# Kernel tuning notes

Hardware: AMD Instinct MI355X
Metric: run time of the kernel (lower is better)

Reference implementation:

```python
import jax, jax.numpy as jnp
import numpy as np

EMB = 768
N_HEADS = 12
HEAD_DIM = EMB // N_HEADS
EPS = 1e-5


def _gelu_tanh(x):
    c = jnp.sqrt(jnp.asarray(2.0 / jnp.pi, x.dtype))
    return 0.5 * x * (1.0 + jnp.tanh(c * (x + 0.044715 * x ** 3)))


def _layernorm(x, scale, shift):
    mean = jnp.mean(x, axis=-1, keepdims=True)
    var = jnp.mean((x - mean) ** 2, axis=-1, keepdims=True)
    return (x - mean) / jnp.sqrt(var + EPS) * scale + shift


def setup_inputs() -> dict:
    key = jax.random.key(0)
    ks = jax.random.split(key, 8)
    s = 0.02  # GPT-2 style init scale
    x = jax.random.normal(ks[0], (8, 1024, EMB), dtype=jnp.float32)
    # torch Linear weights are (out, in); no biases (qkv_bias=False everywhere)
    wq = jax.random.normal(ks[1], (EMB, EMB), dtype=jnp.float32) * s
    wk = jax.random.normal(ks[2], (EMB, EMB), dtype=jnp.float32) * s
    wv = jax.random.normal(ks[3], (EMB, EMB), dtype=jnp.float32) * s
    wo = jax.random.normal(ks[4], (EMB, EMB), dtype=jnp.float32) * s
    w1 = jax.random.normal(ks[5], (4 * EMB, EMB), dtype=jnp.float32) * s
    w2 = jax.random.normal(ks[6], (EMB, 4 * EMB), dtype=jnp.float32) * s
    ln1_scale = jnp.ones((EMB,), jnp.float32)
    ln1_shift = jnp.zeros((EMB,), jnp.float32)
    ln2_scale = jnp.ones((EMB,), jnp.float32)
    ln2_shift = jnp.zeros((EMB,), jnp.float32)
    return dict(x=x, wq=wq, wk=wk, wv=wv, wo=wo, w1=w1, w2=w2,
                ln1_scale=ln1_scale, ln1_shift=ln1_shift,
                ln2_scale=ln2_scale, ln2_shift=ln2_shift)


def reference(x, wq, wk, wv, wo, w1, w2, ln1_scale, ln1_shift, ln2_scale, ln2_shift):
    B, T, E = x.shape
    # --- attention sublayer (pre-LN) ---
    h = _layernorm(x, ln1_scale, ln1_shift)
    q = (h @ wq.T).reshape(B, T, N_HEADS, HEAD_DIM).transpose(0, 2, 1, 3)
    k = (h @ wk.T).reshape(B, T, N_HEADS, HEAD_DIM).transpose(0, 2, 1, 3)
    v = (h @ wv.T).reshape(B, T, N_HEADS, HEAD_DIM).transpose(0, 2, 1, 3)
    scores = jnp.einsum('bhqd,bhkd->bhqk', q, k)  # [B,H,T,T]
    causal = jnp.tril(jnp.ones((T, T), dtype=bool))
    scores = jnp.where(causal, scores, -jnp.inf)
    attn = jax.nn.softmax(scores / np.sqrt(HEAD_DIM), axis=-1)
    ctx = jnp.einsum('bhqk,bhkd->bhqd', attn, v)
    ctx = ctx.transpose(0, 2, 1, 3).reshape(B, T, E)
    x = x + ctx @ wo.T
    # --- FFN sublayer (pre-LN) ---
    h = _layernorm(x, ln2_scale, ln2_shift)
    h = _gelu_tanh(h @ w1.T) @ w2.T
    return x + h
```

## Files before the change

kernel.cpp:

```cpp
#include <hip/hip_runtime.h>
#include <hip/hip_bf16.h>
#include <cstdint>

#define EMB    768
#define NHEADS 12
#define HDIM   64
#define SEQ    1024
#define BATCH  8
#define MROWS  (BATCH*SEQ)
#define FFN    3072
#define W2E    (EMB*EMB)
#define W4E    (FFN*EMB)

typedef __bf16 bf16_t;
typedef bf16_t bf16x8 __attribute__((ext_vector_type(8)));
typedef float  f32x4  __attribute__((ext_vector_type(4)));

__device__ __forceinline__ float b2f(unsigned short u) {
    union { unsigned int i; float f; } t; t.i = ((unsigned int)u) << 16; return t.f;
}
__device__ __forceinline__ unsigned short f2b(float f) {
    union { float f; unsigned int i; } t; t.f = f;
    unsigned int lsb = (t.i >> 16) & 1u;
    t.i += 0x7fffu + lsb;
    return (unsigned short)(t.i >> 16);
}
__device__ __forceinline__ float gelu_f(float x) {
    float u = 0.7978845608028654f * (x + 0.044715f * x * x * x);
    return x * (1.f / (1.f + __expf(-2.f * u)));
}
__device__ __forceinline__ float fexp2(float x) {
#if defined(__has_builtin)
#if __has_builtin(__builtin_amdgcn_exp2f)
    return __builtin_amdgcn_exp2f(x);
#else
    return exp2f(x);
#endif
#else
    return exp2f(x);
#endif
}

#if defined(__has_builtin)
#if __has_builtin(__builtin_amdgcn_global_load_lds)
#define HAS_GLL 1
#endif
#endif
#ifndef HAS_GLL
#define HAS_GLL 0
#endif

__device__ __forceinline__ void gll16(const unsigned short* g, unsigned short* lds_wave_base) {
#if HAS_GLL
    __builtin_amdgcn_global_load_lds(
        (const __attribute__((address_space(1))) unsigned int*)g,
        (__attribute__((address_space(3))) unsigned int*)lds_wave_base, 16, 0, 0);
#endif
}
__device__ __forceinline__ void stage16(const unsigned short* g, unsigned short* lds_wave_base, int lane) {
#if HAS_GLL
    __builtin_amdgcn_global_load_lds(
        (const __attribute__((address_space(1))) unsigned int*)g,
        (__attribute__((address_space(3))) unsigned int*)lds_wave_base, 16, 0, 0);
#else
    *reinterpret_cast<int4*>(lds_wave_base + lane * 8) = *reinterpret_cast<const int4*>(g);
#endif
}

__device__ __forceinline__ int4 load8(const void* src, size_t eoff, bool f32) {
    if (f32) {
        const float4* p = reinterpret_cast<const float4*>((const float*)src + eoff);
        float4 a = p[0], b = p[1];
        union { unsigned short u[8]; int4 v; } r;
        r.u[0] = f2b(a.x); r.u[1] = f2b(a.y); r.u[2] = f2b(a.z); r.u[3] = f2b(a.w);
        r.u[4] = f2b(b.x); r.u[5] = f2b(b.y); r.u[6] = f2b(b.z); r.u[7] = f2b(b.w);
        return r.v;
    }
    return *reinterpret_cast<const int4*>((const unsigned short*)src + eoff);
}
__device__ __forceinline__ float4 load4f(const void* src, size_t eoff, bool f32) {
    if (f32) return *reinterpret_cast<const float4*>((const float*)src + eoff);
    ushort4 u = *reinterpret_cast<const ushort4*>((const unsigned short*)src + eoff);
    float4 r; r.x = b2f(u.x); r.y = b2f(u.y); r.z = b2f(u.z); r.w = b2f(u.w);
    return r;
}

struct DetectArgs { const unsigned short* p[11]; int n[11]; };

__global__ __launch_bounds__(256) void detect_all(DetectArgs a, int* __restrict__ flags) {
    __shared__ int cnt;
    if (threadIdx.x == 0) cnt = 0;
    __syncthreads();
    const unsigned short* src = a.p[blockIdx.x];
    int npairs = a.n[blockIdx.x] / 2;
    if (npairs > 4096) npairs = 4096;
    int local = 0;
    for (int p = threadIdx.x; p < npairs; p += 256) {
        unsigned short u0 = src[2 * p], u1 = src[2 * p + 1];
        int e0 = (u0 >> 7) & 0xFF;
        bool insane0 = (e0 == 0xFF) || (u0 != 0 && (e0 < 96 || e0 > 159));
        bool zpat    = (u0 == 0 && u1 != 0);
        if (insane0 || zpat) ++local;
    }
    atomicAdd(&cnt, local);
    __syncthreads();
    if (threadIdx.x == 0) flags[blockIdx.x] = (cnt * 8 > npairs) ? 1 : 0;
}

__global__ __launch_bounds__(256) void cvt_adapt(
        const void* __restrict__ src, unsigned short* __restrict__ dst,
        int n, const int* __restrict__ flag) {
    int i = blockIdx.x * 256 + threadIdx.x;
    if (i * 4 >= n) return;
    if (*flag) {
        float4 f = reinterpret_cast<const float4*>(src)[i];
        ushort4 o;
        o.x = f2b(f.x); o.y = f2b(f.y); o.z = f2b(f.z); o.w = f2b(f.w);
        reinterpret_cast<ushort4*>(dst)[i] = o;
    } else {
        reinterpret_cast<ushort4*>(dst)[i] = reinterpret_cast<const ushort4*>(src)[i];
    }
}

struct CvtArgs {
    const void* src[6];
    unsigned short* dst[6];
    int n[6];
    int blkoff[7];
    const int* F;
    int fidx[6];
};
__global__ __launch_bounds__(256) void cvt_weights(CvtArgs a) {
    int b = blockIdx.x, seg = 0;
    #pragma unroll
    for (int s = 0; s < 6; ++s) if (b >= a.blkoff[s + 1]) seg = s + 1;
    int i = (b - a.blkoff[seg]) * 256 + threadIdx.x;
    if (i * 4 >= a.n[seg]) return;
    if (a.F[a.fidx[seg]]) {
        float4 f = reinterpret_cast<const float4*>(a.src[seg])[i];
        ushort4 o;
        o.x = f2b(f.x); o.y = f2b(f.y); o.z = f2b(f.z); o.w = f2b(f.w);
        reinterpret_cast<ushort4*>(a.dst[seg])[i] = o;
    } else {
        reinterpret_cast<ushort4*>(a.dst[seg])[i] =
            reinterpret_cast<const ushort4*>(a.src[seg])[i];
    }
}

__global__ __launch_bounds__(256) void reduce2_kernel(
        const float* __restrict__ P, const unsigned short* __restrict__ resid,
        float* __restrict__ out, int n4) {
    int i = blockIdx.x * 256 + threadIdx.x;
    if (i >= n4) return;
    float4 a = reinterpret_cast<const float4*>(P)[i];
    float4 b = reinterpret_cast<const float4*>(P + (size_t)MROWS * EMB)[i];
    ushort4 r = reinterpret_cast<const ushort4*>(resid)[i];
    float4 o;
    o.x = a.x + b.x + b2f(r.x);
    o.y = a.y + b.y + b2f(r.y);
    o.z = a.z + b.z + b2f(r.z);
    o.w = a.w + b.w + b2f(r.w);
    reinterpret_cast<float4*>(out)[i] = o;
}

__global__ __launch_bounds__(256) void ln_kernel(
        const void* __restrict__ x,     const int* __restrict__ fx,
        const void* __restrict__ scale, const int* __restrict__ fsc,
        const void* __restrict__ shift, const int* __restrict__ fsh,
        unsigned short* __restrict__ out) {
    const bool xf = fx && *fx, scf = fsc && *fsc, shf = fsh && *fsh;
    int wave = threadIdx.x >> 6;
    int lane = threadIdx.x & 63;
    int row  = blockIdx.x * 4 + wave;
    const size_t rbase = (size_t)row * EMB;
    float v[12];
    float s = 0.f, s2 = 0.f;
    #pragma unroll
    for (int i = 0; i < 3; ++i) {
        float4 a = load4f(x, rbase + i * 256 + lane * 4, xf);
        v[i*4+0] = a.x; v[i*4+1] = a.y; v[i*4+2] = a.z; v[i*4+3] = a.w;
        s  += a.x + a.y + a.z + a.w;
        s2 += a.x*a.x + a.y*a.y + a.z*a.z + a.w*a.w;
    }
    #pragma unroll
    for (int off = 1; off < 64; off <<= 1) {
        s  += __shfl_xor(s,  off);
        s2 += __shfl_xor(s2, off);
    }
    float mean = s * (1.f / EMB);
    float var  = fmaxf(s2 * (1.f / EMB) - mean * mean, 0.f);
    float rstd = rsqrtf(var + 1e-5f);
    unsigned short* orow = out + rbase;
    #pragma unroll
    for (int i = 0; i < 3; ++i) {
        float4 sc = load4f(scale, i * 256 + lane * 4, scf);
        float4 sh = load4f(shift, i * 256 + lane * 4, shf);
        ushort4 o;
        o.x = f2b((v[i*4+0] - mean) * rstd * sc.x + sh.x);
        o.y = f2b((v[i*4+1] - mean) * rstd * sc.y + sh.y);
        o.z = f2b((v[i*4+2] - mean) * rstd * sc.z + sh.z);
        o.w = f2b((v[i*4+3] - mean) * rstd * sc.w + sh.w);
        *reinterpret_cast<ushort4*>(orow + i * 256 + lane * 4) = o;
    }
}

template<bool GELU, bool RESID, bool OUTF32>
__global__ __launch_bounds__(256) void gemm_lds(
        const unsigned short* __restrict__ A,
        const unsigned short* __restrict__ W,
        const void* R, const int* __restrict__ fR, size_t rOff,
        void* C, int M, int N, int K, int lda, int ldw) {
    constexpr int BK = 32;
    __shared__ __align__(16) unsigned short sA[128 * BK];
    __shared__ __align__(16) unsigned short sB[128 * BK];
    const int m0 = blockIdx.x * 128, n0 = blockIdx.y * 128;
    const int kz = blockIdx.z;
    const int t = threadIdx.x, wave = t >> 6, lane = t & 63;
    const int wrow = (wave >> 1) * 64, wcol = (wave & 1) * 64;
    const int quad = lane >> 4, lr = lane & 15;
    const int r0 = t >> 2;
    const int scg = (t & 3) ^ ((t >> 3) & 3);
    const int c0 = scg * 8;
    const int xq = quad ^ ((lr >> 1) & 3);
    const bool rf = fR && *fR;

    A += (size_t)kz * K;
    W += (size_t)kz * K;

    f32x4 acc[4][4];
    #pragma unroll
    for (int i = 0; i < 4; ++i)
        #pragma unroll
        for (int j = 0; j < 4; ++j)
            acc[i][j] = (f32x4){0.f, 0.f, 0.f, 0.f};

    const unsigned short* gA0 = A + (size_t)(m0 + r0) * lda + c0;
    const unsigned short* gA1 = A + (size_t)(m0 + 64 + r0) * lda + c0;
    const unsigned short* gB0 = W + (size_t)(n0 + r0) * ldw + c0;
    const unsigned short* gB1 = W + (size_t)(n0 + 64 + r0) * ldw + c0;
    unsigned short* lA0 = sA + wave * 512;
    unsigned short* lA1 = sA + 2048 + wave * 512;
    unsigned short* lB0 = sB + wave * 512;
    unsigned short* lB1 = sB + 2048 + wave * 512;

    for (int k0 = 0; k0 < K; k0 += BK) {
#if HAS_GLL
        gll16(gA0 + k0, lA0);
        gll16(gA1 + k0, lA1);
        gll16(gB0 + k0, lB0);
        gll16(gB1 + k0, lB1);
#else
        *reinterpret_cast<int4*>(sA + t * 8)        = *reinterpret_cast<const int4*>(gA0 + k0);
        *reinterpret_cast<int4*>(sA + 2048 + t * 8) = *reinterpret_cast<const int4*>(gA1 + k0);
        *reinterpret_cast<int4*>(sB + t * 8)        = *reinterpret_cast<const int4*>(gB0 + k0);
        *reinterpret_cast<int4*>(sB + 2048 + t * 8) = *reinterpret_cast<const int4*>(gB1 + k0);
#endif
        __syncthreads();
        bf16x8 af[4], bfv[4];
        #pragma unroll
        for (int i = 0; i < 4; ++i)
            af[i] = *reinterpret_cast<const bf16x8*>(
                sA + (wrow >> 6) * 2048 + (i * 16 + lr) * 32 + xq * 8);
        #pragma unroll
        for (int j = 0; j < 4; ++j)
            bfv[j] = *reinterpret_cast<const bf16x8*>(
                sB + (wcol >> 6) * 2048 + (j * 16 + lr) * 32 + xq * 8);
        #pragma unroll
        for (int i = 0; i < 4; ++i)
            #pragma unroll
            for (int j = 0; j < 4; ++j)
                acc[i][j] = __builtin_amdgcn_mfma_f32_16x16x32_bf16(af[i], bfv[j], acc[i][j], 0, 0, 0);
        __syncthreads();
    }

    float* Cf = (float*)C + (size_t)kz * M * N;
    #pragma unroll
    for (int i = 0; i < 4; ++i) {
        #pragma unroll
        for (int j = 0; j < 4; ++j) {
            #pragma unroll
            for (int r = 0; r < 4; ++r) {
                int row = m0 + wrow + i * 16 + quad * 4 + r;
                int col = n0 + wcol + j * 16 + lr;
                float val = acc[i][j][r];
                if (GELU) val = gelu_f(val);
                size_t idx = (size_t)row * N + col;
                if (RESID) {
                    float rv = rf ? ((const float*)R)[idx + rOff]
                                  : b2f(((const unsigned short*)R)[idx + rOff]);
                    val += rv;
                }
                if (OUTF32) Cf[idx] = val;
                else        ((unsigned short*)C)[idx] = f2b(val);
            }
        }
    }
}

template<bool GELU, bool RESID, bool OUTF32>
__global__ __launch_bounds__(256) void gemm_bt(
        const unsigned short* __restrict__ A,
        const void* __restrict__ W, const int* __restrict__ fW,
        const void* R, const int* __restrict__ fR, size_t rOff,
        void* C,
        int M, int N, int K) {
    const bool wf = fW && *fW;
    const bool rf = fR && *fR;
    constexpr int BK = 32, PAD = 8, LDW = BK + PAD;
    __shared__ __align__(16) unsigned short sA[128 * LDW];
    __shared__ __align__(16) unsigned short sB[128 * LDW];
    const int m0 = blockIdx.x * 128;
    const int n0 = blockIdx.y * 128;
    const int t    = threadIdx.x;
    const int wave = t >> 6, lane = t & 63;
    const int wrow = (wave >> 1) * 64, wcol = (wave & 1) * 64;
    const int quad = lane >> 4, lr = lane & 15;
    const int srow = t >> 2, scol = (t & 3) * 8;

    f32x4 acc[4][4];
    #pragma unroll
    for (int i = 0; i < 4; ++i)
        #pragma unroll
        for (int j = 0; j < 4; ++j)
            acc[i][j] = (f32x4){0.f, 0.f, 0.f, 0.f};

    const size_t aBase = (size_t)(m0 + srow) * K + scol;
    const size_t bBase = (size_t)(n0 + srow) * K + scol;

    for (int k0 = 0; k0 < K; k0 += BK) {
        int4 av0 = *reinterpret_cast<const int4*>(A + aBase + k0);
        int4 av1 = *reinterpret_cast<const int4*>(A + aBase + (size_t)64 * K + k0);
        int4 bv0 = load8(W, bBase + k0, wf);
        int4 bv1 = load8(W, bBase + (size_t)64 * K + k0, wf);
        *reinterpret_cast<int4*>(sA + srow * LDW + scol)        = av0;
        *reinterpret_cast<int4*>(sA + (srow + 64) * LDW + scol) = av1;
        *reinterpret_cast<int4*>(sB + srow * LDW + scol)        = bv0;
        *reinterpret_cast<int4*>(sB + (srow + 64) * LDW + scol) = bv1;
        __syncthreads();
        bf16x8 af[4], bfv[4];
        #pragma unroll
        for (int i = 0; i < 4; ++i)
            af[i] = *reinterpret_cast<const bf16x8*>(sA + (wrow + i * 16 + lr) * LDW + quad * 8);
        #pragma unroll
        for (int j = 0; j < 4; ++j)
            bfv[j] = *reinterpret_cast<const bf16x8*>(sB + (wcol + j * 16 + lr) * LDW + quad * 8);
        #pragma unroll
        for (int i = 0; i < 4; ++i)
            #pragma unroll
            for (int j = 0; j < 4; ++j)
                acc[i][j] = __builtin_amdgcn_mfma_f32_16x16x32_bf16(af[i], bfv[j], acc[i][j], 0, 0, 0);
        __syncthreads();
    }

    #pragma unroll
    for (int i = 0; i < 4; ++i) {
        #pragma unroll
        for (int j = 0; j < 4; ++j) {
            #pragma unroll
            for (int r = 0; r < 4; ++r) {
                int row = m0 + wrow + i * 16 + quad * 4 + r;
                int col = n0 + wcol + j * 16 + lr;
                float val = acc[i][j][r];
                if (GELU) val = gelu_f(val);
                size_t idx = (size_t)row * N + col;
                if (RESID) {
                    float rv = rf ? ((const float*)R)[idx + rOff]
                                  : b2f(((const unsigned short*)R)[idx + rOff]);
                    val += rv;
                }
                if (OUTF32) ((float*)C)[idx] = val;
                else        ((unsigned short*)C)[idx] = f2b(val);
            }
        }
    }
}

__global__ __launch_bounds__(256) void fattn_kernel(
        const unsigned short* __restrict__ q,
        const unsigned short* __restrict__ k,
        const unsigned short* __restrict__ v,
        int rs, unsigned short* __restrict__ ctx) {
    constexpr int VTP = 72;
    __shared__ __align__(16) unsigned short sK[2][64 * 64];
    __shared__ __align__(16) unsigned short Vt[2][64 * VTP];
    __shared__ __align__(16) unsigned short Pl[4][16 * VTP];
    const int tid  = threadIdx.x;
    const int wave = tid >> 6, lane = tid & 63;
    const int quad = lane >> 4, lr = lane & 15;
    const int NH   = gridDim.x >> 3;
    const int head = blockIdx.x % NH;
    const int pr   = blockIdx.x / NH;
    const int bb   = head / NHEADS, hd = head % NHEADS;
    const size_t seqbase = (size_t)bb * SEQ;
    constexpr float C2 = 0.18033688011112042f;

    const int krow0 = tid >> 3;
    const int dreal = ((tid & 7) * 8) ^ ((krow0 & 7) << 3);
    const int vrow = tid >> 2;
    const int vcol = (tid & 3) * 16;
    const int vxr  = vrow ^ ((tid & 3) << 4);
    const int kswz = (lr & 7) << 3;
    const int pswr = ((lr >> 2) & 3) << 3;
    unsigned short* Pw = Pl[wave];

    #pragma unroll
    for (int seg = 0; seg < 2; ++seg) {
        const int qt = seg == 0 ? (15 - pr) : pr;
        const int q0 = qt * 64 + wave * 16;

        bf16x8 aQ0, aQ1;
        {
            const unsigned short* qp = q + (seqbase + q0 + lr) * rs + hd * HDIM + quad * 8;
            aQ0 = *reinterpret_cast<const bf16x8*>(qp);
            aQ1 = *reinterpret_cast<const bf16x8*>(qp + 32);
        }

        f32x4 O[4];
        #pragma unroll
        for (int i = 0; i < 4; ++i) O[i] = (f32x4){0.f, 0.f, 0.f, 0.f};
        float mrow[4], lrow[4];
        #pragma unroll
        for (int r = 0; r < 4; ++r) { mrow[r] = -__builtin_inff(); lrow[r] = 0.f; }

        {
            const unsigned short* kp = k + (seqbase + krow0) * rs + hd * HDIM + dreal;
            stage16(kp,                   &sK[0][wave * 512],        lane);
            stage16(kp + (size_t)32 * rs, &sK[0][2048 + wave * 512], lane);
            const unsigned short* vp = v + (seqbase + vrow) * rs + hd * HDIM + vcol;
            union { int4 v4; unsigned short u[8]; } pa, pb;
            pa.v4 = *reinterpret_cast<const int4*>(vp);
            pb.v4 = *reinterpret_cast<const int4*>(vp + 8);
            #pragma unroll
            for (int e = 0; e < 8; ++e) Vt[0][(vcol + e) * VTP + vxr]     = pa.u[e];
            #pragma unroll
            for (int e = 0; e < 8; ++e) Vt[0][(vcol + 8 + e) * VTP + vxr] = pb.u[e];
        }
        __syncthreads();

        for (int kt = 0; kt <= qt; ++kt) {
            const int b = kt & 1;
            union { int4 v4; unsigned short u[8]; } ua, ub;
            if (kt < qt) {
                const unsigned short* kp = k + (seqbase + (size_t)(kt + 1) * 64 + krow0) * rs
                                         + hd * HDIM + dreal;
                stage16(kp,                   &sK[b ^ 1][wave * 512],        lane);
                stage16(kp + (size_t)32 * rs, &sK[b ^ 1][2048 + wave * 512], lane);
                const unsigned short* vp = v + (seqbase + (size_t)(kt + 1) * 64 + vrow) * rs
                                         + hd * HDIM + vcol;
                ua.v4 = *reinterpret_cast<const int4*>(vp);
                ub.v4 = *reinterpret_cast<const int4*>(vp + 8);
            }

            f32x4 S[4];
            #pragma unroll
            for (int sub = 0; sub < 4; ++sub) {
                const unsigned short* kr = &sK[b][(sub * 16 + lr) * 64];
                bf16x8 b0 = *reinterpret_cast<const bf16x8*>(kr + ((quad * 8) ^ kswz));
                bf16x8 b1 = *reinterpret_cast<const bf16x8*>(kr + ((32 + quad * 8) ^ kswz));
                f32x4 accS = (f32x4){0.f, 0.f, 0.f, 0.f};
                accS = __builtin_amdgcn_mfma_f32_16x16x32_bf16(aQ0, b0, accS, 0, 0, 0);
                accS = __builtin_amdgcn_mfma_f32_16x16x32_bf16(aQ1, b1, accS, 0, 0, 0);
                S[sub] = accS;
            }
            const bool diag = (kt == qt);
            #pragma unroll
            for (int sub = 0; sub < 4; ++sub) {
                const int kg = kt * 64 + sub * 16 + lr;
                #pragma unroll
                for (int r = 0; r < 4; ++r) {
                    float s = S[sub][r] * C2;
                    if (diag && kg > q0 + quad * 4 + r) s = -__builtin_inff();
                    S[sub][r] = s;
                }
            }
            float mnew[4], alpha[4];
            #pragma unroll
            for (int r = 0; r < 4; ++r) {
                float mx = fmaxf(fmaxf(S[0][r], S[1][r]), fmaxf(S[2][r], S[3][r]));
                #pragma unroll
                for (int m = 1; m < 16; m <<= 1) mx = fmaxf(mx, __shfl_xor(mx, m));
                mnew[r]  = fmaxf(mrow[r], mx);
                alpha[r] = fexp2(mrow[r] - mnew[r]);
                mrow[r]  = mnew[r];
            }
            float rsum[4] = {0.f, 0.f, 0.f, 0.f};
            #pragma unroll
            for (int sub = 0; sub < 4; ++sub)
                #pragma unroll
                for (int r = 0; r < 4; ++r) {
                    float p = fexp2(S[sub][r] - mnew[r]);
                    S[sub][r] = p;
                    rsum[r] += p;
                }
            #pragma unroll
            for (int r = 0; r < 4; ++r) {
                float rs2 = rsum[r];
                #pragma unroll
                for (int m = 1; m < 16; m <<= 1) rs2 += __shfl_xor(rs2, m);
                lrow[r] = lrow[r] * alpha[r] + rs2;
            }

            #pragma unroll
            for (int sub = 0; sub < 4; ++sub)
                #pragma unroll
                for (int r = 0; r < 4; ++r) {
                    bf16_t hv = (bf16_t)S[sub][r];
                    Pw[(quad * 4 + r) * VTP + ((sub * 16 + lr) ^ (quad << 3))] =
                        *reinterpret_cast<unsigned short*>(&hv);
                }
            if (kt < qt) {
                #pragma unroll
                for (int e = 0; e < 8; ++e) Vt[b ^ 1][(vcol + e) * VTP + vxr]     = ua.u[e];
                #pragma unroll
                for (int e = 0; e < 8; ++e) Vt[b ^ 1][(vcol + 8 + e) * VTP + vxr] = ub.u[e];
            }
            #pragma unroll
            for (int d = 0; d < 4; ++d)
                #pragma unroll
                for (int r = 0; r < 4; ++r)
                    O[d][r] *= alpha[r];

            #pragma unroll
            for (int c = 0; c < 2; ++c) {
                bf16x8 aP = *reinterpret_cast<const bf16x8*>(
                    &Pw[lr * VTP + ((c * 32 + quad * 8) ^ pswr)]);
                #pragma unroll
                for (int d = 0; d < 4; ++d) {
                    bf16x8 bV = *reinterpret_cast<const bf16x8*>(
                        &Vt[b][(d * 16 + lr) * VTP + ((c * 32 + quad * 8) ^ (d << 4))]);
                    O[d] = __builtin_amdgcn_mfma_f32_16x16x32_bf16(aP, bV, O[d], 0, 0, 0);
                }
            }
            __syncthreads();
        }

        #pragma unroll
        for (int r = 0; r < 4; ++r) {
            const float rinv = 1.f / lrow[r];
            const int qg = q0 + quad * 4 + r;
            unsigned short* crow = ctx + (seqbase + qg) * EMB + hd * HDIM;
            #pragma unroll
            for (int d = 0; d < 4; ++d)
                crow[d * 16 + lr] = f2b(O[d][r] * rinv);
        }
    }
}

extern "C" void kernel_launch(void* const* d_in, const int* in_sizes, int n_in,
                              void* d_out, int out_size, void* d_ws, size_t ws_size,
                              hipStream_t stream) {
    const void* x  = d_in[0];
    const void* wq = d_in[1], *wk = d_in[2], *wv = d_in[3], *wo = d_in[4];
    const void* w1 = d_in[5], *w2 = d_in[6];
    const void* g1 = d_in[7], *s1 = d_in[8], *g2 = d_in[9], *s2 = d_in[10];
    char* ws = (char*)d_ws;
    dim3 blk(256);

    int* F = (int*)ws;
    {
        DetectArgs da;
        for (int i = 0; i < 11; ++i) { da.p[i] = (const unsigned short*)d_in[i]; da.n[i] = in_sizes[i]; }
        detect_all<<<11, blk, 0, stream>>>(da, F);
    }

    const size_t SZE = (size_t)MROWS * EMB;
    const size_t SZB = SZE * 2;
    unsigned short* base = (unsigned short*)(ws + 256);
    dim3 g768(MROWS / 128, EMB / 128);

    const size_t FULLB = 256 + 2ULL * (2 * W4E) + 2ULL * (4 * W2E)
                       + 2ULL * ((size_t)MROWS * 2304) + 2 * SZB
                       + 2ULL * ((size_t)MROWS * FFN);
    const size_t FULLB2 = FULLB + 2ULL * SZE * 4;

    if (ws_size >= FULLB2) {
        unsigned short* w1b   = base;
        unsigned short* w2b   = w1b + W4E;
        unsigned short* wqkvb = w2b + W4E;
        unsigned short* wob   = wqkvb + 3 * W2E;
        unsigned short* P     = wob + W2E;
        unsigned short* B0    = P + (size_t)MROWS * 2304;
        unsigned short* B1    = B0 + SZE;
        unsigned short* G     = B1 + SZE;
        float*          PK    = (float*)(G + (size_t)MROWS * FFN);

        {
            CvtArgs ca;
            ca.src[0] = wq; ca.src[1] = wk; ca.src[2] = wv;
            ca.src[3] = wo; ca.src[4] = w1; ca.src[5] = w2;
            ca.dst[0] = wqkvb; ca.dst[1] = wqkvb + W2E; ca.dst[2] = wqkvb + 2 * W2E;
            ca.dst[3] = wob;   ca.dst[4] = w1b;         ca.dst[5] = w2b;
            ca.n[0] = ca.n[1] = ca.n[2] = ca.n[3] = W2E; ca.n[4] = ca.n[5] = W4E;
            int off = 0;
            for (int s = 0; s < 6; ++s) { ca.blkoff[s] = off; off += ca.n[s] / 1024; }
            ca.blkoff[6] = off;
            ca.F = F;
            ca.fidx[0] = 1; ca.fidx[1] = 2; ca.fidx[2] = 3;
            ca.fidx[3] = 4; ca.fidx[4] = 5; ca.fidx[5] = 6;
            cvt_weights<<<off, blk, 0, stream>>>(ca);
        }

        ln_kernel<<<MROWS / 4, blk, 0, stream>>>(x, F+0, g1, F+7, s1, F+8, B1);
        dim3 gqkv(MROWS / 128, 2304 / 128);
        gemm_lds<false, false, false><<<gqkv, blk, 0, stream>>>(B1, wqkvb, nullptr, nullptr, 0, P, MROWS, 2304, EMB, EMB, EMB);
        fattn_kernel<<<BATCH * NHEADS * 8, blk, 0, stream>>>(P, P + 768, P + 1536, 2304, B0);
        gemm_lds<false, true, false><<<g768, blk, 0, stream>>>(B0, wob, x, F+0, 0, B1, MROWS, EMB, EMB, EMB, EMB);
        ln_kernel<<<MROWS / 4, blk, 0, stream>>>(B1, nullptr, g2, F+9, s2, F+10, B0);
        dim3 gffn1(MROWS / 128, FFN / 128);
        gemm_lds<true, false, false><<<gffn1, blk, 0, stream>>>(B0, w1b, nullptr, nullptr, 0, G, MROWS, FFN, EMB, EMB, EMB);
        dim3 gsk(MROWS / 128, EMB / 128, 2);
        gemm_lds<false, false, true><<<gsk, blk, 0, stream>>>(G, w2b, nullptr, nullptr, 0, PK, MROWS, EMB, FFN / 2, FFN, FFN);
        reduce2_kernel<<<(SZE / 4 + 255) / 256, blk, 0, stream>>>(PK, B1, (float*)d_out, SZE / 4);
    } else if (ws_size >= FULLB) {
        unsigned short* w1b   = base;
        unsigned short* w2b   = w1b + W4E;
        unsigned short* wqkvb = w2b + W4E;
        unsigned short* wob   = wqkvb + 3 * W2E;
        unsigned short* P     = wob + W2E;
        unsigned short* B0    = P + (size_t)MROWS * 2304;
        unsigned short* B1    = B0 + SZE;
        unsigned short* G     = B1 + SZE;

        {
            CvtArgs ca;
            ca.src[0] = wq; ca.src[1] = wk; ca.src[2] = wv;
            ca.src[3] = wo; ca.src[4] = w1; ca.src[5] = w2;
            ca.dst[0] = wqkvb; ca.dst[1] = wqkvb + W2E; ca.dst[2] = wqkvb + 2 * W2E;
            ca.dst[3] = wob;   ca.dst[4] = w1b;         ca.dst[5] = w2b;
            ca.n[0] = ca.n[1] = ca.n[2] = ca.n[3] = W2E; ca.n[4] = ca.n[5] = W4E;
            int off = 0;
            for (int s = 0; s < 6; ++s) { ca.blkoff[s] = off; off += ca.n[s] / 1024; }
            ca.blkoff[6] = off;
            ca.F = F;
            ca.fidx[0] = 1; ca.fidx[1] = 2; ca.fidx[2] = 3;
            ca.fidx[3] = 4; ca.fidx[4] = 5; ca.fidx[5] = 6;
            cvt_weights<<<off, blk, 0, stream>>>(ca);
        }

        ln_kernel<<<MROWS / 4, blk, 0, stream>>>(x, F+0, g1, F+7, s1, F+8, B1);
        dim3 gqkv(MROWS / 128, 2304 / 128);
        gemm_lds<false, false, false><<<gqkv, blk, 0, stream>>>(B1, wqkvb, nullptr, nullptr, 0, P, MROWS, 2304, EMB, EMB, EMB);
        fattn_kernel<<<BATCH * NHEADS * 8, blk, 0, stream>>>(P, P + 768, P + 1536, 2304, B0);
        gemm_lds<false, true, false><<<g768, blk, 0, stream>>>(B0, wob, x, F+0, 0, B1, MROWS, EMB, EMB, EMB, EMB);
        ln_kernel<<<MROWS / 4, blk, 0, stream>>>(B1, nullptr, g2, F+9, s2, F+10, B0);
        dim3 gffn1(MROWS / 128, FFN / 128);
        gemm_lds<true, false, false><<<gffn1, blk, 0, stream>>>(B0, w1b, nullptr, nullptr, 0, G, MROWS, FFN, EMB, EMB, EMB);
        gemm_lds<false, true, true><<<g768, blk, 0, stream>>>(G, w2b, B1, nullptr, 0, d_out, MROWS, EMB, FFN, FFN, FFN);
    } else if (ws_size >= 256 + 4 * SZB) {
        unsigned short* B0 = base;
        unsigned short* B1 = B0 + SZE;
        unsigned short* B2 = B1 + SZE;
        unsigned short* B3 = B2 + SZE;
        ln_kernel<<<MROWS / 4, blk, 0, stream>>>(x, F+0, g1, F+7, s1, F+8, B0);
        gemm_bt<false, false, false><<<g768, blk, 0, stream>>>(B0, wq, F+1, nullptr, nullptr, 0, B1, MROWS, EMB, EMB);
        gemm_bt<false, false, false><<<g768, blk, 0, stream>>>(B0, wk, F+2, nullptr, nullptr, 0, B2, MROWS, EMB, EMB);
        gemm_bt<false, false, false><<<g768, blk, 0, stream>>>(B0, wv, F+3, nullptr, nullptr, 0, B3, MROWS, EMB, EMB);
        fattn_kernel<<<BATCH * NHEADS * 8, blk, 0, stream>>>(B1, B2, B3, EMB, B0);
        gemm_bt<false, true, false><<<g768, blk, 0, stream>>>(B0, wo, F+4, x, F+0, 0, B1, MROWS, EMB, EMB);
        ln_kernel<<<MROWS / 4, blk, 0, stream>>>(B1, nullptr, g2, F+9, s2, F+10, B2);
        dim3 c3072(2048 / 128, FFN / 128), c768(2048 / 128, EMB / 128);
        for (int c = 0; c < 4; ++c) {
            const size_t r0 = (size_t)c * 2048;
            gemm_bt<true, false, false><<<c3072, blk, 0, stream>>>(B2 + r0 * EMB, w1, F+5, nullptr, nullptr, 0, B3, 2048, FFN, EMB);
            gemm_bt<false, true, true><<<c768, blk, 0, stream>>>(B3, w2, F+6, B1 + r0 * EMB, nullptr, 0, (float*)d_out + r0 * EMB, 2048, EMB, FFN);
        }
    } else {
        unsigned short* hlow = (unsigned short*)d_out;
        unsigned short* x2up = (unsigned short*)d_out + SZE;
        unsigned short* wsQ = base;
        unsigned short* wsK = wsQ + (size_t)1024 * EMB;
        unsigned short* wsV = wsK + (size_t)1024 * EMB;
        unsigned short* wsC = wsV + (size_t)1024 * EMB;
        ln_kernel<<<MROWS / 4, blk, 0, stream>>>(x, F+0, g1, F+7, s1, F+8, hlow);
        dim3 q768(1024 / 128, EMB / 128);
        for (int grp = 0; grp < BATCH; ++grp) {
            const size_t r0 = (size_t)grp * 1024;
            gemm_bt<false, false, false><<<q768, blk, 0, stream>>>(hlow + r0 * EMB, wq, F+1, nullptr, nullptr, 0, wsQ, 1024, EMB, EMB);
            gemm_bt<false, false, false><<<q768, blk, 0, stream>>>(hlow + r0 * EMB, wk, F+2, nullptr, nullptr, 0, wsK, 1024, EMB, EMB);
            gemm_bt<false, false, false><<<q768, blk, 0, stream>>>(hlow + r0 * EMB, wv, F+3, nullptr, nullptr, 0, wsV, 1024, EMB, EMB);
            fattn_kernel<<<1 * NHEADS * 8, blk, 0, stream>>>(wsQ, wsK, wsV, EMB, wsC);
            gemm_bt<false, true, false><<<q768, blk, 0, stream>>>(wsC, wo, F+4, x, F+0, r0 * EMB, x2up + r0 * EMB, 1024, EMB, EMB);
        }
        unsigned short* xb = base;
        unsigned short* h2 = xb + (size_t)1024 * EMB;
        unsigned short* gb = h2 + (size_t)1024 * EMB;
        dim3 f3072(1024 / 128, FFN / 128), f768(1024 / 128, EMB / 128);
        for (int c = 0; c < BATCH; ++c) {
            const size_t r0 = (size_t)c * 1024;
            hipMemcpyAsync(xb, x2up + r0 * EMB, (size_t)1024 * EMB * 2,
                           hipMemcpyDeviceToDevice, stream);
            ln_kernel<<<1024 / 4, blk, 0, stream>>>(xb, nullptr, g2, F+9, s2, F+10, h2);
            gemm_bt<true, false, false><<<f3072, blk, 0, stream>>>(h2, w1, F+5, nullptr, nullptr, 0, gb, 1024, FFN, EMB);
            gemm_bt<false, true, true><<<f768, blk, 0, stream>>>(gb, w2, F+6, xb, nullptr, 0, (float*)d_out + r0 * EMB, 1024, EMB, FFN);
        }
    }
}
```

Before: 402.3 us.

## Double-buffer LDS in gemm_lds and use faster exp2/rcp GELU

Double-buffers the shared-memory tiles in gemm_lds so the next K-slice is prefetched (via global_load_lds when available) while MFMAs run on the current one, and drops one barrier per iteration. It also adds a launch-bounds occupancy hint, rewrites GELU with exp2 plus a hardware reciprocal, and uses the native bf16 conversion for stores. The extra LDS buffer doubles shared-memory use, and the single barrier per iteration may leave a race when the async LDS writes for the next slice are not waited on before the following compute.

Measured after the change: 390.6 us. -2.9%, faster.

```diff
diff --git a/kernel.cpp b/kernel.cpp
--- a/kernel.cpp
+++ b/kernel.cpp
@@ -25,10 +25,6 @@
     t.i += 0x7fffu + lsb;
     return (unsigned short)(t.i >> 16);
 }
-__device__ __forceinline__ float gelu_f(float x) {
-    float u = 0.7978845608028654f * (x + 0.044715f * x * x * x);
-    return x * (1.f / (1.f + __expf(-2.f * u)));
-}
 __device__ __forceinline__ float fexp2(float x) {
 #if defined(__has_builtin)
 #if __has_builtin(__builtin_amdgcn_exp2f)
@@ -39,6 +35,22 @@
 #else
     return exp2f(x);
 #endif
+}
+__device__ __forceinline__ float frcp(float x) {
+#if defined(__has_builtin)
+#if __has_builtin(__builtin_amdgcn_rcpf)
+    return __builtin_amdgcn_rcpf(x);
+#else
+    return 1.f / x;
+#endif
+#else
+    return 1.f / x;
+#endif
+}
+__device__ __forceinline__ float gelu_f(float x) {
+    float x2 = x * x;
+    float u  = x * __builtin_fmaf(x2, -0.10294823f, -2.3022082f);
+    return x * frcp(1.f + fexp2(u));
 }
 
 #if defined(__has_builtin)
@@ -205,17 +217,18 @@
 }
 
 template<bool GELU, bool RESID, bool OUTF32>
-__global__ __launch_bounds__(256) void gemm_lds(
+__global__ __launch_bounds__(256, 3) void gemm_lds(
         const unsigned short* __restrict__ A,
         const unsigned short* __restrict__ W,
         const void* R, const int* __restrict__ fR, size_t rOff,
         void* C, int M, int N, int K, int lda, int ldw) {
     constexpr int BK = 32;
-    __shared__ __align__(16) unsigned short sA[128 * BK];
-    __shared__ __align__(16) unsigned short sB[128 * BK];
+    __shared__ __align__(16) unsigned short sA[2][128 * BK];
+    __shared__ __align__(16) unsigned short sB[2][128 * BK];
     const int m0 = blockIdx.x * 128, n0 = blockIdx.y * 128;
     const int kz = blockIdx.z;
-    const int t = threadIdx.x, wave = t >> 6, lane = t & 63;
+    const int t = threadIdx.x, wave = t >> 6;
+    const int lane = t & 63;
     const int wrow = (wave >> 1) * 64, wcol = (wave & 1) * 64;
     const int quad = lane >> 4, lr = lane & 15;
     const int r0 = t >> 2;
@@ -238,39 +251,53 @@
     const unsigned short* gA1 = A + (size_t)(m0 + 64 + r0) * lda + c0;
     const unsigned short* gB0 = W + (size_t)(n0 + r0) * ldw + c0;
     const unsigned short* gB1 = W + (size_t)(n0 + 64 + r0) * ldw + c0;
-    unsigned short* lA0 = sA + wave * 512;
-    unsigned short* lA1 = sA + 2048 + wave * 512;
-    unsigned short* lB0 = sB + wave * 512;
-    unsigned short* lB1 = sB + 2048 + wave * 512;
-
+
+#if HAS_GLL
+    gll16(gA0, sA[0] + wave * 512);
+    gll16(gA1, sA[0] + 2048 + wave * 512);
+    gll16(gB0, sB[0] + wave * 512);
+    gll16(gB1, sB[0] + 2048 + wave * 512);
+#else
+    *reinterpret_cast<int4*>(sA[0] + t * 8)        = *reinterpret_cast<const int4*>(gA0);
+    *reinterpret_cast<int4*>(sA[0] + 2048 + t * 8) = *reinterpret_cast<const int4*>(gA1);
+    *reinterpret_cast<int4*>(sB[0] + t * 8)        = *reinterpret_cast<const int4*>(gB0);
+    *reinterpret_cast<int4*>(sB[0] + 2048 + t * 8) = *reinterpret_cast<const int4*>(gB1);
+#endif
+    __syncthreads();
+
+    int buf = 0;
     for (int k0 = 0; k0 < K; k0 += BK) {
+        if (k0 + BK < K) {
+            const int pf = buf ^ 1;
+            const int kn = k0 + BK;
 #if HAS_GLL
-        gll16(gA0 + k0, lA0);
-        gll16(gA1 + k0, lA1);
-        gll16(gB0 + k0, lB0);
-        gll16(gB1 + k0, lB1);
+            gll16(gA0 + kn, sA[pf] + wave * 512);
+            gll16(gA1 + kn, sA[pf] + 2048 + wave * 512);
+            gll16(gB0 + kn, sB[pf] + wave * 512);
+            gll16(gB1 + kn, sB[pf] + 2048 + wave * 512);
 #else
-        *reinterpret_cast<int4*>(sA + t * 8)        = *reinterpret_cast<const int4*>(gA0 + k0);
-        *reinterpret_cast<int4*>(sA + 2048 + t * 8) = *reinterpret_cast<const int4*>(gA1 + k0);
-        *reinterpret_cast<int4*>(sB + t * 8)        = *reinterpret_cast<const int4*>(gB0 + k0);
-        *reinterpret_cast<int4*>(sB + 2048 + t * 8) = *reinterpret_cast<const int4*>(gB1 + k0);
-#endif
-        __syncthreads();
+            *reinterpret_cast<int4*>(sA[pf] + t * 8)        = *reinterpret_cast<const int4*>(gA0 + kn);
+            *reinterpret_cast<int4*>(sA[pf] + 2048 + t * 8) = *reinterpret_cast<const int4*>(gA1 + kn);
+            *reinterpret_cast<int4*>(sB[pf] + t * 8)        = *reinterpret_cast<const int4*>(gB0 + kn);
+            *reinterpret_cast<int4*>(sB[pf] + 2048 + t * 8) = *reinterpret_cast<const int4*>(gB1 + kn);
+#endif
+        }
         bf16x8 af[4], bfv[4];
         #pragma unroll
         for (int i = 0; i < 4; ++i)
             af[i] = *reinterpret_cast<const bf16x8*>(
-                sA + (wrow >> 6) * 2048 + (i * 16 + lr) * 32 + xq * 8);
+                sA[buf] + (wrow >> 6) * 2048 + (i * 16 + lr) * 32 + xq * 8);
         #pragma unroll
         for (int j = 0; j < 4; ++j)
             bfv[j] = *reinterpret_cast<const bf16x8*>(
-                sB + (wcol >> 6) * 2048 + (j * 16 + lr) * 32 + xq * 8);
+                sB[buf] + (wcol >> 6) * 2048 + (j * 16 + lr) * 32 + xq * 8);
         #pragma unroll
         for (int i = 0; i < 4; ++i)
             #pragma unroll
             for (int j = 0; j < 4; ++j)
                 acc[i][j] = __builtin_amdgcn_mfma_f32_16x16x32_bf16(af[i], bfv[j], acc[i][j], 0, 0, 0);
         __syncthreads();
+        buf ^= 1;
     }
 
     float* Cf = (float*)C + (size_t)kz * M * N;
@@ -291,7 +318,10 @@
                     val += rv;
                 }
                 if (OUTF32) Cf[idx] = val;
-                else        ((unsigned short*)C)[idx] = f2b(val);
+                else {
+                    bf16_t hv = (bf16_t)val;
+                    ((unsigned short*)C)[idx] = *reinterpret_cast<unsigned short*>(&hv);
+                }
             }
         }
     }
```
